# Optimization experiments

Measured on AMD Instinct MI355X. Metric: run time of the kernel, lower is better.

Reference implementation:

```python
import jax, jax.numpy as jnp
import numpy as np

K = 1024  # number of superpixels (spx.max()+1 in the original)

def setup_inputs() -> dict:
    key = jax.random.key(0)
    k1, k2 = jax.random.split(key)
    img = jax.random.normal(k1, (4, 128, 512, 512), dtype=jnp.float32)
    spx = jax.random.randint(k2, (4, 512, 512), 0, K, dtype=jnp.int32)
    return {"img": img, "spx": spx}

def _segment_max_one(img_b, spx_b):
    # img_b: [C, H, W], spx_b: [H, W]
    C = img_b.shape[0]
    data = img_b.reshape(C, -1).T          # [HW, C]
    ids = spx_b.reshape(-1)                # [HW]
    out = jax.ops.segment_max(data, ids, num_segments=K)  # [K, C]
    return out.T                           # [C, K]

def reference(img, spx):
    # Max-pool features over superpixel segments: output [B, C, K]
    return jax.vmap(_segment_max_one)(img, spx)
```

## Files before the change

### kernel.cpp

```cpp
#include <hip/hip_runtime.h>

#define KSEG   1024
#define CCH    128
#define HWPIX  (512 * 512)
#define BB     4
#define BLOCK  256
#define W      8192
#define CGRP   32
#define LITERS (W / (BLOCK * 4))

#define ORD_NEG_INF ((int)0x807FFFFF)

__device__ __forceinline__ int ord_f32(float f) {
    int i = __float_as_int(f);
    return i >= 0 ? i : (i ^ 0x7FFFFFFF);
}

__global__ __launch_bounds__(BLOCK) void init_kernel(int* __restrict__ out) {
    out[blockIdx.x * BLOCK + threadIdx.x] = ORD_NEG_INF;
}

__global__ __launch_bounds__(BLOCK) void decode_kernel(int* __restrict__ out) {
    const int idx = blockIdx.x * BLOCK + threadIdx.x;
    const int i = out[idx];
    ((float*)out)[idx] = __int_as_float(i >= 0 ? i : (i ^ 0x7FFFFFFF));
}

__global__ __launch_bounds__(BLOCK) void pool_kernel(const float* __restrict__ img,
                                                     const int* __restrict__ spx,
                                                     int* __restrict__ out) {
    __shared__ unsigned short sidx[W];
    __shared__ int start[KSEG + 1];
    __shared__ int cursor[KSEG];
    __shared__ __align__(16) float buf[W];
    __shared__ int scanbuf[BLOCK];

    const int tid = threadIdx.x;
    const int b   = blockIdx.z;
    const int c0  = blockIdx.y * CGRP;
    const int wx  = blockIdx.x * W;
    const int* __restrict__ spx_w = spx + b * HWPIX + wx;
    const float* __restrict__ img_w = img + ((size_t)(b * CCH + c0)) * HWPIX + wx;

    for (int i = tid; i < KSEG; i += BLOCK) cursor[i] = 0;
    __syncthreads();

    for (int it = 0; it < LITERS; ++it) {
        const int4 id = *(const int4*)(spx_w + (it * BLOCK + tid) * 4);
        atomicAdd(&cursor[id.x], 1);
        atomicAdd(&cursor[id.y], 1);
        atomicAdd(&cursor[id.z], 1);
        atomicAdd(&cursor[id.w], 1);
    }
    __syncthreads();

    int loc[4], s0 = 0;
#pragma unroll
    for (int j = 0; j < 4; ++j) { loc[j] = s0; s0 += cursor[tid * 4 + j]; }
    scanbuf[tid] = s0;
    __syncthreads();
    for (int off = 1; off < BLOCK; off <<= 1) {
        const int v = (tid >= off) ? scanbuf[tid - off] : 0;
        __syncthreads();
        scanbuf[tid] += v;
        __syncthreads();
    }
    const int base = scanbuf[tid] - s0;
#pragma unroll
    for (int j = 0; j < 4; ++j) {
        start[tid * 4 + j]  = base + loc[j];
        cursor[tid * 4 + j] = base + loc[j];
    }
    if (tid == 0) start[KSEG] = W;
    __syncthreads();

    for (int it = 0; it < LITERS; ++it) {
        const int p = (it * BLOCK + tid) * 4;
        const int4 id = *(const int4*)(spx_w + p);
        sidx[atomicAdd(&cursor[id.x], 1)] = (unsigned short)(p);
        sidx[atomicAdd(&cursor[id.y], 1)] = (unsigned short)(p + 1);
        sidx[atomicAdd(&cursor[id.z], 1)] = (unsigned short)(p + 2);
        sidx[atomicAdd(&cursor[id.w], 1)] = (unsigned short)(p + 3);
    }
    __syncthreads();

    int rs[4], re[4];
#pragma unroll
    for (int q = 0; q < 4; ++q) {
        rs[q] = start[tid + q * BLOCK];
        re[q] = start[tid + q * BLOCK + 1];
    }

    const float NEG_INF = __int_as_float(0xFF800000);

    float4 r[LITERS];
#pragma unroll
    for (int it = 0; it < LITERS; ++it)
        r[it] = *(const float4*)(img_w + (size_t)0 * HWPIX + (it * BLOCK + tid) * 4);

    for (int c = 0; c < CGRP; ++c) {
        __syncthreads();
#pragma unroll
        for (int it = 0; it < LITERS; ++it)
            *(float4*)&buf[(it * BLOCK + tid) * 4] = r[it];
        if (c + 1 < CGRP) {
            const float* __restrict__ src = img_w + (size_t)(c + 1) * HWPIX;
#pragma unroll
            for (int it = 0; it < LITERS; ++it)
                r[it] = *(const float4*)(src + (it * BLOCK + tid) * 4);
        }
        __syncthreads();

        int* __restrict__ outc = out + ((size_t)(b * CCH + c0 + c)) * KSEG;
#pragma unroll
        for (int q = 0; q < 4; ++q) {
            const int s = tid + q * BLOCK;
            float m = NEG_INF;
            int i = rs[q];
            const int e = re[q];
            for (; i + 4 <= e; i += 4) {
                const int i0 = sidx[i], i1 = sidx[i + 1], i2 = sidx[i + 2], i3 = sidx[i + 3];
                const float a = buf[i0], bb2 = buf[i1], cc = buf[i2], dd = buf[i3];
                m = fmaxf(m, fmaxf(fmaxf(a, bb2), fmaxf(cc, dd)));
            }
            for (; i < e; ++i) m = fmaxf(m, buf[sidx[i]]);
            atomicMax(&outc[s], ord_f32(m));
        }
    }
}

extern "C" void kernel_launch(void* const* d_in, const int* in_sizes, int n_in,
                              void* d_out, int out_size, void* d_ws, size_t ws_size,
                              hipStream_t stream) {
    const float* img = (const float*)d_in[0];
    const int*   spx = (const int*)d_in[1];
    int* out = (int*)d_out;

    init_kernel<<<out_size / BLOCK, BLOCK, 0, stream>>>(out);

    dim3 grid(HWPIX / W, CCH / CGRP, BB);
    pool_kernel<<<grid, BLOCK, 0, stream>>>(img, spx, out);

    decode_kernel<<<out_size / BLOCK, BLOCK, 0, stream>>>(out);
}
```

Before: 804.6 us.

## Scatter pixels into segment-sorted shared buffer instead of gathering via index list

Each thread now stores the destination slot for each of its 32 pixels in registers, computed during the counting-sort pass. Every channel's pixels are scattered straight into segment order in shared memory. The per-segment max then reads contiguous memory with float2 loads instead of a two-level sidx-then-buf gather. The channel group shrinks from 32 to 16, which doubles the block count and the global atomicMax traffic. It also adds register pressure from the 32-entry dst array plus the ids array, and the scattered shared-memory writes may cause bank conflicts.

```diff
diff --git a/kernel.cpp b/kernel.cpp
--- a/kernel.cpp
+++ b/kernel.cpp
@@ -6,7 +6,8 @@
 #define BB     4
 #define BLOCK  256
 #define W      8192
-#define CGRP   32
+#define CGRP   16
+#define PPT    (W / BLOCK)
 #define LITERS (W / (BLOCK * 4))
 
 #define ORD_NEG_INF ((int)0x807FFFFF)
@@ -29,10 +30,9 @@
 __global__ __launch_bounds__(BLOCK) void pool_kernel(const float* __restrict__ img,
                                                      const int* __restrict__ spx,
                                                      int* __restrict__ out) {
-    __shared__ unsigned short sidx[W];
+    __shared__ __align__(16) float buf[W];
     __shared__ int start[KSEG + 1];
     __shared__ int cursor[KSEG];
-    __shared__ __align__(16) float buf[W];
     __shared__ int scanbuf[BLOCK];
 
     const int tid = threadIdx.x;
@@ -45,12 +45,14 @@
     for (int i = tid; i < KSEG; i += BLOCK) cursor[i] = 0;
     __syncthreads();
 
+    int4 ids[LITERS];
+#pragma unroll
     for (int it = 0; it < LITERS; ++it) {
-        const int4 id = *(const int4*)(spx_w + (it * BLOCK + tid) * 4);
-        atomicAdd(&cursor[id.x], 1);
-        atomicAdd(&cursor[id.y], 1);
-        atomicAdd(&cursor[id.z], 1);
-        atomicAdd(&cursor[id.w], 1);
+        ids[it] = *(const int4*)(spx_w + (it * BLOCK + tid) * 4);
+        atomicAdd(&cursor[ids[it].x], 1);
+        atomicAdd(&cursor[ids[it].y], 1);
+        atomicAdd(&cursor[ids[it].z], 1);
+        atomicAdd(&cursor[ids[it].w], 1);
     }
     __syncthreads();
 
@@ -74,15 +76,14 @@
     if (tid == 0) start[KSEG] = W;
     __syncthreads();
 
+    int dst[PPT];
+#pragma unroll
     for (int it = 0; it < LITERS; ++it) {
-        const int p = (it * BLOCK + tid) * 4;
-        const int4 id = *(const int4*)(spx_w + p);
-        sidx[atomicAdd(&cursor[id.x], 1)] = (unsigned short)(p);
-        sidx[atomicAdd(&cursor[id.y], 1)] = (unsigned short)(p + 1);
-        sidx[atomicAdd(&cursor[id.z], 1)] = (unsigned short)(p + 2);
-        sidx[atomicAdd(&cursor[id.w], 1)] = (unsigned short)(p + 3);
+        dst[it * 4 + 0] = atomicAdd(&cursor[ids[it].x], 1);
+        dst[it * 4 + 1] = atomicAdd(&cursor[ids[it].y], 1);
+        dst[it * 4 + 2] = atomicAdd(&cursor[ids[it].z], 1);
+        dst[it * 4 + 3] = atomicAdd(&cursor[ids[it].w], 1);
     }
-    __syncthreads();
 
     int rs[4], re[4];
 #pragma unroll
@@ -96,13 +97,17 @@
     float4 r[LITERS];
 #pragma unroll
     for (int it = 0; it < LITERS; ++it)
-        r[it] = *(const float4*)(img_w + (size_t)0 * HWPIX + (it * BLOCK + tid) * 4);
+        r[it] = *(const float4*)(img_w + (it * BLOCK + tid) * 4);
 
     for (int c = 0; c < CGRP; ++c) {
         __syncthreads();
 #pragma unroll
-        for (int it = 0; it < LITERS; ++it)
-            *(float4*)&buf[(it * BLOCK + tid) * 4] = r[it];
+        for (int it = 0; it < LITERS; ++it) {
+            buf[dst[it * 4 + 0]] = r[it].x;
+            buf[dst[it * 4 + 1]] = r[it].y;
+            buf[dst[it * 4 + 2]] = r[it].z;
+            buf[dst[it * 4 + 3]] = r[it].w;
+        }
         if (c + 1 < CGRP) {
             const float* __restrict__ src = img_w + (size_t)(c + 1) * HWPIX;
 #pragma unroll
@@ -115,15 +120,15 @@
 #pragma unroll
         for (int q = 0; q < 4; ++q) {
             const int s = tid + q * BLOCK;
-            float m = NEG_INF;
             int i = rs[q];
             const int e = re[q];
-            for (; i + 4 <= e; i += 4) {
-                const int i0 = sidx[i], i1 = sidx[i + 1], i2 = sidx[i + 2], i3 = sidx[i + 3];
-                const float a = buf[i0], bb2 = buf[i1], cc = buf[i2], dd = buf[i3];
-                m = fmaxf(m, fmaxf(fmaxf(a, bb2), fmaxf(cc, dd)));
+            float m = NEG_INF;
+            if ((i & 1) && i < e) m = buf[i++];
+            for (; i + 2 <= e; i += 2) {
+                const float2 v = *(const float2*)&buf[i];
+                m = fmaxf(m, fmaxf(v.x, v.y));
             }
-            for (; i < e; ++i) m = fmaxf(m, buf[sidx[i]]);
+            if (i < e) m = fmaxf(m, buf[i]);
             atomicMax(&outc[s], ord_f32(m));
         }
     }
```

Measured after the change: 731.6 us. 1.1x faster.
